# Optimization experiments

Measured on AMD Instinct MI355X. Metric: run time of the kernel, lower is better.

The kernel has to match this reference:

```python
import jax, jax.numpy as jnp
import numpy as np

H, B, T, DH = 16, 2, 2048, 64
MODEL_DIM = 1024


def setup_inputs() -> dict:
    key = jax.random.key(0)
    ks = jax.random.split(key, 5)
    q = jax.random.normal(ks[0], (H, B, T, DH), dtype=jnp.float32)
    k = jax.random.normal(ks[1], (H, B, T, DH), dtype=jnp.float32)
    v = jax.random.normal(ks[2], (H, B, T, DH), dtype=jnp.float32)
    Wo_w = jax.random.normal(ks[3], (MODEL_DIM, H * DH), dtype=jnp.float32) * 0.02
    Wo_b = jax.random.normal(ks[4], (MODEL_DIM,), dtype=jnp.float32) * 0.02
    return {"q": q, "k": k, "v": v, "Wo_w": Wo_w, "Wo_b": Wo_b}


def reference(q, k, v, Wo_w, Wo_b):
    # per-head scaled dot-product attention; scale uses per-head dk (=DH)
    scale = jnp.sqrt(jnp.asarray(DH, dtype=q.dtype))
    # scores: [H, B, T, T]
    scores = jnp.einsum('hbtd,hbsd->hbts', q, k) / scale
    # causal mask (additive -1e12 on strict upper triangle, matching torch code)
    mask = jnp.triu(jnp.ones((T, T), dtype=bool), 1)
    scores = scores + (-1e12) * mask.astype(scores.dtype)
    weights = jax.nn.softmax(scores, axis=-1)
    # context per head: [H, B, T, DH]
    context = jnp.einsum('hbts,hbsd->hbtd', weights, v)
    # concat heads along feature dim: [B, T, H*DH]
    context = jnp.transpose(context, (1, 2, 0, 3)).reshape(B, T, H * DH)
    # output projection (torch Linear: x @ W.T + b)
    return context @ Wo_w.T + Wo_b
```

## Files before the change

kernel.cpp:

```cpp
#include <hip/hip_runtime.h>

typedef __attribute__((ext_vector_type(8))) short bf16x8;
typedef __attribute__((ext_vector_type(4))) float f32x4;
typedef __attribute__((ext_vector_type(4))) unsigned int u32x4;
typedef __attribute__((ext_vector_type(4))) unsigned short u16x4;

#define H_ 16
#define B_ 2
#define T_ 2048
#define DH_ 64
#define MD_ 1024

static __device__ inline unsigned short f2bf(float f) {
    union { float f; unsigned u; } x; x.f = f;
    unsigned r = (x.u + 0x7fffu + ((x.u >> 16) & 1u)) >> 16;
    return (unsigned short)r;
}
static __device__ inline unsigned int pack_bf2(float lo, float hi) {
    return __builtin_amdgcn_perm(__float_as_uint(hi), __float_as_uint(lo), 0x07060302u);
}
static __device__ inline unsigned short hi16(float f) {
    return (unsigned short)(__float_as_uint(f) >> 16);
}
static __device__ inline float fexp2(float x) {
#if __has_builtin(__builtin_amdgcn_exp2f)
    return __builtin_amdgcn_exp2f(x);
#else
    return exp2f(x);
#endif
}

__global__ __launch_bounds__(256) void prep_k(const float* __restrict__ k,
                                              const float* __restrict__ v,
                                              const float* __restrict__ w,
                                              unsigned short* __restrict__ kb,
                                              unsigned short* __restrict__ vtb,
                                              unsigned short* __restrict__ wob,
                                              int* __restrict__ fl) {
    __shared__ __attribute__((aligned(16))) unsigned short vt64[64][64];
    const int blk = blockIdx.x;
    const int tid = threadIdx.x;
    if (blk < 1024) {
        int i = (blk * 256 + tid) * 4;
        f32x4 x = *(const f32x4*)(w + i);
        u16x4 y;
        y[0] = f2bf(x[0]); y[1] = f2bf(x[1]); y[2] = f2bf(x[2]); y[3] = f2bf(x[3]);
        *(u16x4*)(wob + i) = y;
    } else if (blk < 2048) {
        int j = blk - 1024;
        const int hb = j >> 5, s0 = (j & 31) * 64;
        const int row = tid >> 2, c = (tid & 3) * 16;
        const long off = (long)hb * (T_ * DH_) + (long)(s0 + row) * DH_ + c;
        const float* p = k + off;
        f32x4 a0 = *(const f32x4*)p;
        f32x4 a1 = *(const f32x4*)(p + 4);
        f32x4 a2 = *(const f32x4*)(p + 8);
        f32x4 a3 = *(const f32x4*)(p + 12);
        u32x4 w0, w1;
        w0[0] = pack_bf2(a0[0], a0[1]); w0[1] = pack_bf2(a0[2], a0[3]);
        w0[2] = pack_bf2(a1[0], a1[1]); w0[3] = pack_bf2(a1[2], a1[3]);
        w1[0] = pack_bf2(a2[0], a2[1]); w1[1] = pack_bf2(a2[2], a2[3]);
        w1[2] = pack_bf2(a3[0], a3[1]); w1[3] = pack_bf2(a3[2], a3[3]);
        *(u32x4*)(kb + off) = w0;
        *(u32x4*)(kb + off + 8) = w1;
    } else if (blk < 3072) {
        int j = blk - 2048;
        const int hb = j >> 5, s0 = (j & 31) * 64;
        const int vkp = tid & 31, vdg = tid >> 5;
        const float* vp = v + (long)hb * (T_ * DH_) + (long)(s0 + 2 * vkp) * DH_ + vdg * 8;
        f32x4 va0 = *(const f32x4*)vp;
        f32x4 va1 = *(const f32x4*)(vp + 4);
        f32x4 vb0 = *(const f32x4*)(vp + DH_);
        f32x4 vb1 = *(const f32x4*)(vp + DH_ + 4);
#pragma unroll
        for (int jj = 0; jj < 4; jj++) {
            ((unsigned int*)&vt64[vdg * 8 + jj][0])[vkp]     = pack_bf2(va0[jj], vb0[jj]);
            ((unsigned int*)&vt64[vdg * 8 + 4 + jj][0])[vkp] = pack_bf2(va1[jj], vb1[jj]);
        }
        __syncthreads();
        const int dh = tid >> 2, kc = (tid & 3) * 16;
        u32x4 o0 = *(const u32x4*)&vt64[dh][kc];
        u32x4 o1 = *(const u32x4*)&vt64[dh][kc + 8];
        unsigned short* op = vtb + (long)hb * (DH_ * T_) + (long)dh * T_ + s0 + kc;
        *(u32x4*)op = o0;
        *(u32x4*)(op + 8) = o1;
    } else {
        for (int z = tid; z < 512; z += 256) fl[z] = 0;
    }
}

#define SE(t, lo, hi) ((unsigned)((t) | ((lo) << 8) | ((hi) << 16)))
__constant__ unsigned sched48[48] = {
    SE(31,0,16), SE(31,16,32), SE(30,15,31), SE(15,0,16),
    SE(30,0,15), SE(29,0,15), SE(29,15,30), SE(28,14,29), SE(14,0,15),
    SE(28,0,14), SE(27,0,14), SE(27,14,28), SE(26,13,27), SE(13,0,14),
    SE(26,0,13), SE(25,0,13), SE(25,13,26), SE(24,12,25), SE(12,0,13),
    SE(24,0,12), SE(23,0,12), SE(23,12,24), SE(22,11,23), SE(11,0,12),
    SE(22,0,11), SE(21,0,11), SE(21,11,22), SE(20,10,21), SE(10,0,11),
    SE(20,0,10), SE(19,0,10), SE(19,10,20), SE(18,9,19), SE(9,0,10),
    SE(18,0,9), SE(17,0,9), SE(17,9,18), SE(16,8,17), SE(8,0,9),
    SE(16,0,8), SE(7,0,8),
    SE(6,0,7), SE(5,0,6), SE(4,0,5), SE(3,0,4), SE(2,0,3), SE(1,0,2), SE(0,0,1)
};

__global__ __launch_bounds__(256, 4) void attn_k(const float* __restrict__ q,
                                                 const unsigned short* __restrict__ kb,
                                                 const unsigned short* __restrict__ vtb,
                                                 unsigned short* __restrict__ ctx,
                                                 float* __restrict__ Op,
                                                 float* __restrict__ lp,
                                                 int* __restrict__ fl) {
    const int i = blockIdx.x;
    const int xcd = i & 7, j = i >> 3;
    const int l = j & 3, idx = j >> 2;
    const unsigned e = sched48[idx];
    const int t  = (int)(e & 255u);
    const int lo = (int)((e >> 8) & 255u);
    const int hi = (int)(e >> 16);
    const int hb = xcd * 4 + l;
    const int h = hb >> 1, b = hb & 1;
    const int tid = threadIdx.x;
    const int wave = tid >> 6, lane = tid & 63;
    const int ln = lane & 15, quad = lane >> 4;

    __shared__ __attribute__((aligned(16))) unsigned short kt[64][72];
    __shared__ __attribute__((aligned(16))) unsigned short vt[64][72];
    __shared__ __attribute__((aligned(16))) unsigned short pl[4][16][72];
    __shared__ int sh_who;

    const long kbase = (long)hb * (T_ * DH_);
    const long vbase = (long)hb * (DH_ * T_);
    const int q0w = t * 64 + wave * 16;
    const int srow = tid >> 2, sc = (tid & 3) * 16;

    bf16x8 ones;
#pragma unroll
    for (int z = 0; z < 8; z++) ones[z] = (short)0x3F80;

    bf16x8 qf0, qf1;
    {
        const float qs = 0.18033688011112042f;
        const float* qp = q + kbase + (long)(q0w + ln) * DH_ + quad * 8;
        f32x4 a0 = *(const f32x4*)qp;
        f32x4 a1 = *(const f32x4*)(qp + 4);
        f32x4 b0 = *(const f32x4*)(qp + 32);
        f32x4 b1 = *(const f32x4*)(qp + 36);
#pragma unroll
        for (int z = 0; z < 4; z++) {
            qf0[z]   = (short)f2bf(a0[z] * qs);
            qf0[4+z] = (short)f2bf(a1[z] * qs);
            qf1[z]   = (short)f2bf(b0[z] * qs);
            qf1[4+z] = (short)f2bf(b1[z] * qs);
        }
    }

    f32x4 oacc[4];
#pragma unroll
    for (int z = 0; z < 4; z++) oacc[z] = f32x4{0.f, 0.f, 0.f, 0.f};
    f32x4 lacc = f32x4{0.f, 0.f, 0.f, 0.f};

    u32x4 kr0, kr1, vr0, vr1;
    {
        const unsigned short* kp = kb + kbase + (long)(lo * 64 + srow) * DH_ + sc;
        kr0 = *(const u32x4*)kp; kr1 = *(const u32x4*)(kp + 8);
        const unsigned short* vp = vtb + vbase + (long)srow * T_ + lo * 64 + sc;
        vr0 = *(const u32x4*)vp; vr1 = *(const u32x4*)(vp + 8);
    }

#pragma unroll 1
    for (int step = lo; step < hi; step++) {
        __syncthreads();
        *(u32x4*)&kt[srow][sc]     = kr0;
        *(u32x4*)&kt[srow][sc + 8] = kr1;
        *(u32x4*)&vt[srow][sc]     = vr0;
        *(u32x4*)&vt[srow][sc + 8] = vr1;
        __syncthreads();

        if (step + 1 < hi) {
            const unsigned short* kp = kb + kbase + (long)((step + 1) * 64 + srow) * DH_ + sc;
            kr0 = *(const u32x4*)kp; kr1 = *(const u32x4*)(kp + 8);
            const unsigned short* vp = vtb + vbase + (long)srow * T_ + (step + 1) * 64 + sc;
            vr0 = *(const u32x4*)vp; vr1 = *(const u32x4*)(vp + 8);
        }

        f32x4 sa[4];
#pragma unroll
        for (int nt = 0; nt < 4; nt++) {
            bf16x8 kf0 = *(const bf16x8*)&kt[nt * 16 + ln][quad * 8];
            bf16x8 kf1 = *(const bf16x8*)&kt[nt * 16 + ln][32 + quad * 8];
            f32x4 a = f32x4{0.f, 0.f, 0.f, 0.f};
            a = __builtin_amdgcn_mfma_f32_16x16x32_bf16(qf0, kf0, a, 0, 0, 0);
            a = __builtin_amdgcn_mfma_f32_16x16x32_bf16(qf1, kf1, a, 0, 0, 0);
            sa[nt] = a;
        }

        if (step == t) {
            const int lr = wave * 16 + quad * 4;
#pragma unroll
            for (int nt = 0; nt < 4; nt++)
#pragma unroll
                for (int r = 0; r < 4; r++) {
                    float p = fexp2(sa[nt][r]);
                    if (nt * 16 + ln > lr + r) p = 0.f;
                    pl[wave][quad * 4 + r][nt * 16 + ln] = hi16(p);
                }
        } else {
#pragma unroll
            for (int nt = 0; nt < 4; nt++)
#pragma unroll
                for (int r = 0; r < 4; r++)
                    pl[wave][quad * 4 + r][nt * 16 + ln] = hi16(fexp2(sa[nt][r]));
        }

        bf16x8 pf0 = *(const bf16x8*)&pl[wave][ln][quad * 8];
        bf16x8 pf1 = *(const bf16x8*)&pl[wave][ln][32 + quad * 8];

#pragma unroll
        for (int dt = 0; dt < 4; dt++) {
            bf16x8 vf0 = *(const bf16x8*)&vt[dt * 16 + ln][quad * 8];
            bf16x8 vf1 = *(const bf16x8*)&vt[dt * 16 + ln][32 + quad * 8];
            oacc[dt] = __builtin_amdgcn_mfma_f32_16x16x32_bf16(pf0, vf0, oacc[dt], 0, 0, 0);
            oacc[dt] = __builtin_amdgcn_mfma_f32_16x16x32_bf16(pf1, vf1, oacc[dt], 0, 0, 0);
        }
        lacc = __builtin_amdgcn_mfma_f32_16x16x32_bf16(pf0, ones, lacc, 0, 0, 0);
        lacc = __builtin_amdgcn_mfma_f32_16x16x32_bf16(pf1, ones, lacc, 0, 0, 0);
    }

    if (t < 16) {
#pragma unroll
        for (int r = 0; r < 4; r++) {
            float rl = __builtin_amdgcn_rcpf(lacc[r]);
            int row_g = q0w + quad * 4 + r;
#pragma unroll
            for (int dt = 0; dt < 4; dt++)
                ctx[(long)(b * T_ + row_g) * MD_ + h * 64 + dt * 16 + ln] =
                    f2bf(oacc[dt][r] * rl);
        }
    } else {
        const int c = (lo != 0) ? 1 : 0;
        const long prow = (long)(t - 16) * 64 + wave * 16 + quad * 4;
        const long pbase = (((long)c * 32 + hb) * 1024 + prow) * 64 + ln;
#pragma unroll
        for (int r = 0; r < 4; r++)
#pragma unroll
            for (int dt = 0; dt < 4; dt++)
                __hip_atomic_store(&Op[pbase + (long)r * 64 + dt * 16], oacc[dt][r],
                                   __ATOMIC_RELAXED, __HIP_MEMORY_SCOPE_AGENT);
        if (ln == 0) {
#pragma unroll
            for (int r = 0; r < 4; r++)
                __hip_atomic_store(&lp[((long)c * 32 + hb) * 1024 + prow + r], lacc[r],
                                   __ATOMIC_RELAXED, __HIP_MEMORY_SCOPE_AGENT);
        }
        __syncthreads();
        if (tid == 0)
            sh_who = __hip_atomic_fetch_add(&fl[hb * 16 + (t - 16)], 1,
                                            __ATOMIC_RELAXED, __HIP_MEMORY_SCOPE_AGENT);
        __syncthreads();
        if (sh_who == 1) {
            const long qbase = (((long)(c ^ 1) * 32 + hb) * 1024 + prow) * 64 + ln;
#pragma unroll
            for (int r = 0; r < 4; r++) {
#pragma unroll
                for (int dt = 0; dt < 4; dt++)
                    oacc[dt][r] += __hip_atomic_load(&Op[qbase + (long)r * 64 + dt * 16],
                                                     __ATOMIC_RELAXED, __HIP_MEMORY_SCOPE_AGENT);
                lacc[r] += __hip_atomic_load(&lp[((long)(c ^ 1) * 32 + hb) * 1024 + prow + r],
                                             __ATOMIC_RELAXED, __HIP_MEMORY_SCOPE_AGENT);
            }
#pragma unroll
            for (int r = 0; r < 4; r++) {
                float rl = __builtin_amdgcn_rcpf(lacc[r]);
                int row_g = q0w + quad * 4 + r;
#pragma unroll
                for (int dt = 0; dt < 4; dt++)
                    ctx[(long)(b * T_ + row_g) * MD_ + h * 64 + dt * 16 + ln] =
                        f2bf(oacc[dt][r] * rl);
            }
        }
    }
}

__global__ __launch_bounds__(256, 4) void proj_k(const unsigned short* __restrict__ A,
                                                 const unsigned short* __restrict__ Bw,
                                                 const float* __restrict__ bias,
                                                 float* __restrict__ out) {
    const int i = blockIdx.x;
    const int n0 = ((i & 7) * 2 + ((i >> 3) & 1)) * 64;
    const int m0 = (i >> 4) * 64;
    const int tid = threadIdx.x;
    const int wave = tid >> 6, lane = tid & 63;
    const int ln = lane & 15, quad = lane >> 4;

    __shared__ __attribute__((aligned(16))) unsigned short As[64][72];
    __shared__ __attribute__((aligned(16))) unsigned short Bs[64][72];

    const int srow = tid >> 2, sc = (tid & 3) * 16;

    f32x4 acc[4];
#pragma unroll
    for (int z = 0; z < 4; z++) acc[z] = f32x4{0.f, 0.f, 0.f, 0.f};

    u32x4 ar0, ar1, br0, br1;
    {
        const unsigned short* ap = A + (long)(m0 + srow) * 1024 + sc;
        ar0 = *(const u32x4*)ap; ar1 = *(const u32x4*)(ap + 8);
        const unsigned short* bp = Bw + (long)(n0 + srow) * 1024 + sc;
        br0 = *(const u32x4*)bp; br1 = *(const u32x4*)(bp + 8);
    }

#pragma unroll 1
    for (int ks = 0; ks < 1024; ks += 64) {
        __syncthreads();
        *(u32x4*)&As[srow][sc]     = ar0;
        *(u32x4*)&As[srow][sc + 8] = ar1;
        *(u32x4*)&Bs[srow][sc]     = br0;
        *(u32x4*)&Bs[srow][sc + 8] = br1;
        __syncthreads();

        if (ks + 64 < 1024) {
            const unsigned short* ap = A + (long)(m0 + srow) * 1024 + ks + 64 + sc;
            ar0 = *(const u32x4*)ap; ar1 = *(const u32x4*)(ap + 8);
            const unsigned short* bp = Bw + (long)(n0 + srow) * 1024 + ks + 64 + sc;
            br0 = *(const u32x4*)bp; br1 = *(const u32x4*)(bp + 8);
        }

        bf16x8 bf0 = *(const bf16x8*)&Bs[wave * 16 + ln][quad * 8];
        bf16x8 bf1 = *(const bf16x8*)&Bs[wave * 16 + ln][32 + quad * 8];
#pragma unroll
        for (int mt = 0; mt < 4; mt++) {
            bf16x8 af0 = *(const bf16x8*)&As[mt * 16 + ln][quad * 8];
            bf16x8 af1 = *(const bf16x8*)&As[mt * 16 + ln][32 + quad * 8];
            acc[mt] = __builtin_amdgcn_mfma_f32_16x16x32_bf16(af0, bf0, acc[mt], 0, 0, 0);
            acc[mt] = __builtin_amdgcn_mfma_f32_16x16x32_bf16(af1, bf1, acc[mt], 0, 0, 0);
        }
    }

    int col = n0 + wave * 16 + ln;
    float bz = bias[col];
#pragma unroll
    for (int mt = 0; mt < 4; mt++)
#pragma unroll
        for (int r = 0; r < 4; r++) {
            int row = m0 + mt * 16 + quad * 4 + r;
            out[(long)row * 1024 + col] = acc[mt][r] + bz;
        }
}

extern "C" void kernel_launch(void* const* d_in, const int* in_sizes, int n_in,
                              void* d_out, int out_size, void* d_ws, size_t ws_size,
                              hipStream_t stream) {
    const float* q    = (const float*)d_in[0];
    const float* k    = (const float*)d_in[1];
    const float* v    = (const float*)d_in[2];
    const float* Wo_w = (const float*)d_in[3];
    const float* Wo_b = (const float*)d_in[4];
    float* out = (float*)d_out;

    unsigned short* ctx = (unsigned short*)d_ws;
    unsigned short* wob = ctx + (size_t)4096 * 1024;
    unsigned short* kbb = wob + (size_t)1024 * 1024;
    unsigned short* vtb = kbb + (size_t)32 * 2048 * 64;
    float* Opart = (float*)(vtb + (size_t)32 * 2048 * 64);
    float* lpart = Opart + (size_t)2 * 32 * 1024 * 64;
    int*   flags = (int*)(lpart + (size_t)2 * 32 * 1024);

    prep_k<<<3073, 256, 0, stream>>>(k, v, Wo_w, kbb, vtb, wob, flags);
    attn_k<<<1536, 256, 0, stream>>>(q, kbb, vtb, ctx, Opart, lpart, flags);
    proj_k<<<1024, 256, 0, stream>>>(ctx, wob, Wo_b, out);
}
```

Baseline: 152.5 us.

## Compute transposed score and output tiles to vectorize P writes and drop row-sum MFMA

Swaps MFMA operand order so each lane holds a query column of S^T and O^T. The P tile can then be written to LDS as packed 8-byte bf16 stores instead of 16 scalar 2-byte stores. The row sum is accumulated in registers with two cross-lane shuffles at the end, replacing two extra MFMAs per step against a ones vector. Epilogue stores become 4-wide bf16 writes. This adds a few VALU adds per step and changes P rounding from truncation to perm-based packing.

```diff
diff --git a/kernel.cpp b/kernel.cpp
--- a/kernel.cpp
+++ b/kernel.cpp
@@ -3,6 +3,7 @@
 typedef __attribute__((ext_vector_type(8))) short bf16x8;
 typedef __attribute__((ext_vector_type(4))) float f32x4;
 typedef __attribute__((ext_vector_type(4))) unsigned int u32x4;
+typedef __attribute__((ext_vector_type(2))) unsigned int u32x2;
 typedef __attribute__((ext_vector_type(4))) unsigned short u16x4;
 
 #define H_ 16
@@ -18,9 +19,6 @@
 }
 static __device__ inline unsigned int pack_bf2(float lo, float hi) {
     return __builtin_amdgcn_perm(__float_as_uint(hi), __float_as_uint(lo), 0x07060302u);
-}
-static __device__ inline unsigned short hi16(float f) {
-    return (unsigned short)(__float_as_uint(f) >> 16);
 }
 static __device__ inline float fexp2(float x) {
 #if __has_builtin(__builtin_amdgcn_exp2f)
@@ -133,10 +131,6 @@
     const int q0w = t * 64 + wave * 16;
     const int srow = tid >> 2, sc = (tid & 3) * 16;
 
-    bf16x8 ones;
-#pragma unroll
-    for (int z = 0; z < 8; z++) ones[z] = (short)0x3F80;
-
     bf16x8 qf0, qf1;
     {
         const float qs = 0.18033688011112042f;
@@ -154,10 +148,10 @@
         }
     }
 
-    f32x4 oacc[4];
-#pragma unroll
-    for (int z = 0; z < 4; z++) oacc[z] = f32x4{0.f, 0.f, 0.f, 0.f};
-    f32x4 lacc = f32x4{0.f, 0.f, 0.f, 0.f};
+    f32x4 oT[4];
+#pragma unroll
+    for (int z = 0; z < 4; z++) oT[z] = f32x4{0.f, 0.f, 0.f, 0.f};
+    float lsum = 0.f;
 
     u32x4 kr0, kr1, vr0, vr1;
     {
@@ -189,27 +183,39 @@
             bf16x8 kf0 = *(const bf16x8*)&kt[nt * 16 + ln][quad * 8];
             bf16x8 kf1 = *(const bf16x8*)&kt[nt * 16 + ln][32 + quad * 8];
             f32x4 a = f32x4{0.f, 0.f, 0.f, 0.f};
-            a = __builtin_amdgcn_mfma_f32_16x16x32_bf16(qf0, kf0, a, 0, 0, 0);
-            a = __builtin_amdgcn_mfma_f32_16x16x32_bf16(qf1, kf1, a, 0, 0, 0);
+            a = __builtin_amdgcn_mfma_f32_16x16x32_bf16(kf0, qf0, a, 0, 0, 0);
+            a = __builtin_amdgcn_mfma_f32_16x16x32_bf16(kf1, qf1, a, 0, 0, 0);
             sa[nt] = a;
         }
 
         if (step == t) {
-            const int lr = wave * 16 + quad * 4;
+            const int qi = wave * 16 + ln;
 #pragma unroll
             for (int nt = 0; nt < 4; nt++)
 #pragma unroll
                 for (int r = 0; r < 4; r++) {
                     float p = fexp2(sa[nt][r]);
-                    if (nt * 16 + ln > lr + r) p = 0.f;
-                    pl[wave][quad * 4 + r][nt * 16 + ln] = hi16(p);
+                    if (nt * 16 + quad * 4 + r > qi) p = 0.f;
+                    sa[nt][r] = p;
                 }
         } else {
 #pragma unroll
             for (int nt = 0; nt < 4; nt++)
 #pragma unroll
                 for (int r = 0; r < 4; r++)
-                    pl[wave][quad * 4 + r][nt * 16 + ln] = hi16(fexp2(sa[nt][r]));
+                    sa[nt][r] = fexp2(sa[nt][r]);
+        }
+
+#pragma unroll
+        for (int nt = 0; nt < 4; nt++)
+            lsum += (sa[nt][0] + sa[nt][1]) + (sa[nt][2] + sa[nt][3]);
+
+#pragma unroll
+        for (int nt = 0; nt < 4; nt++) {
+            u32x2 ww;
+            ww[0] = pack_bf2(sa[nt][0], sa[nt][1]);
+            ww[1] = pack_bf2(sa[nt][2], sa[nt][3]);
+            *(u32x2*)&pl[wave][ln][nt * 16 + quad * 4] = ww;
         }
 
         bf16x8 pf0 = *(const bf16x8*)&pl[wave][ln][quad * 8];
@@ -219,63 +225,60 @@
         for (int dt = 0; dt < 4; dt++) {
             bf16x8 vf0 = *(const bf16x8*)&vt[dt * 16 + ln][quad * 8];
             bf16x8 vf1 = *(const bf16x8*)&vt[dt * 16 + ln][32 + quad * 8];
-            oacc[dt] = __builtin_amdgcn_mfma_f32_16x16x32_bf16(pf0, vf0, oacc[dt], 0, 0, 0);
-            oacc[dt] = __builtin_amdgcn_mfma_f32_16x16x32_bf16(pf1, vf1, oacc[dt], 0, 0, 0);
-        }
-        lacc = __builtin_amdgcn_mfma_f32_16x16x32_bf16(pf0, ones, lacc, 0, 0, 0);
-        lacc = __builtin_amdgcn_mfma_f32_16x16x32_bf16(pf1, ones, lacc, 0, 0, 0);
-    }
+            oT[dt] = __builtin_amdgcn_mfma_f32_16x16x32_bf16(vf0, pf0, oT[dt], 0, 0, 0);
+            oT[dt] = __builtin_amdgcn_mfma_f32_16x16x32_bf16(vf1, pf1, oT[dt], 0, 0, 0);
+        }
+    }
+
+    lsum += __shfl_xor(lsum, 16);
+    lsum += __shfl_xor(lsum, 32);
+
+    const int row_g = q0w + ln;
 
     if (t < 16) {
-#pragma unroll
-        for (int r = 0; r < 4; r++) {
-            float rl = __builtin_amdgcn_rcpf(lacc[r]);
-            int row_g = q0w + quad * 4 + r;
-#pragma unroll
-            for (int dt = 0; dt < 4; dt++)
-                ctx[(long)(b * T_ + row_g) * MD_ + h * 64 + dt * 16 + ln] =
-                    f2bf(oacc[dt][r] * rl);
+        float rl = __builtin_amdgcn_rcpf(lsum);
+#pragma unroll
+        for (int dt = 0; dt < 4; dt++) {
+            u16x4 y;
+            y[0] = f2bf(oT[dt][0] * rl); y[1] = f2bf(oT[dt][1] * rl);
+            y[2] = f2bf(oT[dt][2] * rl); y[3] = f2bf(oT[dt][3] * rl);
+            *(u16x4*)&ctx[(long)(b * T_ + row_g) * MD_ + h * 64 + dt * 16 + quad * 4] = y;
         }
     } else {
         const int c = (lo != 0) ? 1 : 0;
-        const long prow = (long)(t - 16) * 64 + wave * 16 + quad * 4;
-        const long pbase = (((long)c * 32 + hb) * 1024 + prow) * 64 + ln;
-#pragma unroll
-        for (int r = 0; r < 4; r++)
-#pragma unroll
-            for (int dt = 0; dt < 4; dt++)
-                __hip_atomic_store(&Op[pbase + (long)r * 64 + dt * 16], oacc[dt][r],
+        const long prow = (long)(t - 16) * 64 + wave * 16 + ln;
+        const long pbase = (((long)c * 32 + hb) * 1024 + prow) * 64;
+#pragma unroll
+        for (int dt = 0; dt < 4; dt++)
+#pragma unroll
+            for (int r = 0; r < 4; r++)
+                __hip_atomic_store(&Op[pbase + dt * 16 + quad * 4 + r], oT[dt][r],
                                    __ATOMIC_RELAXED, __HIP_MEMORY_SCOPE_AGENT);
-        if (ln == 0) {
-#pragma unroll
-            for (int r = 0; r < 4; r++)
-                __hip_atomic_store(&lp[((long)c * 32 + hb) * 1024 + prow + r], lacc[r],
-                                   __ATOMIC_RELAXED, __HIP_MEMORY_SCOPE_AGENT);
-        }
+        if (quad == 0)
+            __hip_atomic_store(&lp[((long)c * 32 + hb) * 1024 + prow], lsum,
+                               __ATOMIC_RELAXED, __HIP_MEMORY_SCOPE_AGENT);
         __syncthreads();
         if (tid == 0)
             sh_who = __hip_atomic_fetch_add(&fl[hb * 16 + (t - 16)], 1,
                                             __ATOMIC_RELAXED, __HIP_MEMORY_SCOPE_AGENT);
         __syncthreads();
         if (sh_who == 1) {
-            const long qbase = (((long)(c ^ 1) * 32 + hb) * 1024 + prow) * 64 + ln;
-#pragma unroll
-            for (int r = 0; r < 4; r++) {
-#pragma unroll
-                for (int dt = 0; dt < 4; dt++)
-                    oacc[dt][r] += __hip_atomic_load(&Op[qbase + (long)r * 64 + dt * 16],
-                                                     __ATOMIC_RELAXED, __HIP_MEMORY_SCOPE_AGENT);
-                lacc[r] += __hip_atomic_load(&lp[((long)(c ^ 1) * 32 + hb) * 1024 + prow + r],
-                                             __ATOMIC_RELAXED, __HIP_MEMORY_SCOPE_AGENT);
-            }
-#pragma unroll
-            for (int r = 0; r < 4; r++) {
-                float rl = __builtin_amdgcn_rcpf(lacc[r]);
-                int row_g = q0w + quad * 4 + r;
-#pragma unroll
-                for (int dt = 0; dt < 4; dt++)
-                    ctx[(long)(b * T_ + row_g) * MD_ + h * 64 + dt * 16 + ln] =
-                        f2bf(oacc[dt][r] * rl);
+            const long qbase = (((long)(c ^ 1) * 32 + hb) * 1024 + prow) * 64;
+#pragma unroll
+            for (int dt = 0; dt < 4; dt++)
+#pragma unroll
+                for (int r = 0; r < 4; r++)
+                    oT[dt][r] += __hip_atomic_load(&Op[qbase + dt * 16 + quad * 4 + r],
+                                                   __ATOMIC_RELAXED, __HIP_MEMORY_SCOPE_AGENT);
+            lsum += __hip_atomic_load(&lp[((long)(c ^ 1) * 32 + hb) * 1024 + prow],
+                                      __ATOMIC_RELAXED, __HIP_MEMORY_SCOPE_AGENT);
+            float rl = __builtin_amdgcn_rcpf(lsum);
+#pragma unroll
+            for (int dt = 0; dt < 4; dt++) {
+                u16x4 y;
+                y[0] = f2bf(oT[dt][0] * rl); y[1] = f2bf(oT[dt][1] * rl);
+                y[2] = f2bf(oT[dt][2] * rl); y[3] = f2bf(oT[dt][3] * rl);
+                *(u16x4*)&ctx[(long)(b * T_ + row_g) * MD_ + h * 64 + dt * 16 + quad * 4] = y;
             }
         }
     }
```

Result: slower. 167.0 us (+9.5%).
